# Kernel optimization log

Measured on AMD Instinct MI355X. Metric: run time of the kernel, lower is better.

The kernel has to match this reference:

```python
import jax, jax.numpy as jnp
import numpy as np

NU, NI, E = 100000, 100000, 500000  # users, items, edges per edge type
DIN, DH, DOUT = 128, 256, 128


def setup_inputs() -> dict:
    key = jax.random.key(0)
    ks = jax.random.split(key, 18)
    f = lambda k, s: jax.random.normal(k, s, dtype=jnp.float32) * 0.02
    inp = {
        # node embedding tables (x_dict defaults to embedding weights)
        'emb_user': f(ks[0], (NU, DIN)),
        'emb_item': f(ks[1], (NI, DIN)),
        # conv1 params: relation user->item (dst=item) and item->user (dst=user)
        'W1_self_ui': f(ks[2], (DIN, DH)), 'W1_neigh_ui': f(ks[3], (DIN, DH)), 'b1_ui': jnp.zeros((DH,), jnp.float32),
        'W1_self_iu': f(ks[4], (DIN, DH)), 'W1_neigh_iu': f(ks[5], (DIN, DH)), 'b1_iu': jnp.zeros((DH,), jnp.float32),
        # conv2 params
        'W2_self_ui': f(ks[6], (DH, DOUT)), 'W2_neigh_ui': f(ks[7], (DH, DOUT)), 'b2_ui': jnp.zeros((DOUT,), jnp.float32),
        'W2_self_iu': f(ks[8], (DH, DOUT)), 'W2_neigh_iu': f(ks[9], (DH, DOUT)), 'b2_iu': jnp.zeros((DOUT,), jnp.float32),
        # edge lists: e1 = user->item edges, e2 = item->user edges
        'e1_src': jax.random.randint(ks[10], (E,), 0, NU),
        'e1_dst': jax.random.randint(ks[11], (E,), 0, NI),
        'e2_src': jax.random.randint(ks[12], (E,), 0, NI),
        'e2_dst': jax.random.randint(ks[13], (E,), 0, NU),
    }
    return inp


def _sage(h_src, h_dst, e_src, e_dst, W_self, W_neigh, b, n_dst):
    # DGL SAGEConv('mean'): fc_self(h_dst) + fc_neigh(mean_neighbors(h_src)) + bias
    msg = h_src[e_src]                                   # [E, d] gather
    ssum = jax.ops.segment_sum(msg, e_dst, num_segments=n_dst)          # [n_dst, d]
    deg = jax.ops.segment_sum(jnp.ones((e_src.shape[0], 1), h_src.dtype), e_dst, num_segments=n_dst)
    mean = ssum / jnp.maximum(deg, 1.0)                  # zero in-degree -> 0
    return h_dst @ W_self + mean @ W_neigh + b


def reference(emb_user, emb_item,
              W1_self_ui, W1_neigh_ui, b1_ui, W1_self_iu, W1_neigh_iu, b1_iu,
              W2_self_ui, W2_neigh_ui, b2_ui, W2_self_iu, W2_neigh_iu, b2_iu,
              e1_src, e1_dst, e2_src, e2_dst):
    # layer 1 (HeteroGraphConv: each ntype receives from exactly one relation)
    h1_item = jax.nn.leaky_relu(_sage(emb_user, emb_item, e1_src, e1_dst, W1_self_ui, W1_neigh_ui, b1_ui, NI))
    h1_user = jax.nn.leaky_relu(_sage(emb_item, emb_user, e2_src, e2_dst, W1_self_iu, W1_neigh_iu, b1_iu, NU))
    # layer 2
    h2_item = _sage(h1_user, h1_item, e1_src, e1_dst, W2_self_ui, W2_neigh_ui, b2_ui, NI)
    h2_user = _sage(h1_item, h1_user, e2_src, e2_dst, W2_self_iu, W2_neigh_iu, b2_iu, NU)
    return (h2_user, h2_item)
```

## Files before the change

kernel.cpp:

```cpp
#include <hip/hip_runtime.h>
#include <stdint.h>

typedef unsigned short u16;
typedef unsigned int   u32;
typedef __attribute__((ext_vector_type(8))) short bf16x8;
typedef __attribute__((ext_vector_type(4))) float f32x4;
typedef __attribute__((ext_vector_type(2))) float f32x2;
typedef __attribute__((ext_vector_type(8))) unsigned short u16x8;

constexpr int NUc = 100000;
constexpr int NIc = 100000;
constexpr int Ec  = 500000;
constexpr int Mrows = 100000;
constexpr int NB  = (100000 + 255) / 256;

__device__ __forceinline__ u16 f2bf(float f) {
  u32 u = __float_as_uint(f);
  u += 0x7fffu + ((u >> 16) & 1u);
  return (u16)(u >> 16);
}
__device__ __forceinline__ float bf2f(u16 h) { return __uint_as_float(((u32)h) << 16); }

constexpr int PREP_B = 4096;
constexpr int HIST_B = 1024;
__global__ void prep_hist(const float* __restrict__ eu, const float* __restrict__ ei,
                          const float* __restrict__ W1s_ui, const float* __restrict__ W1n_ui,
                          const float* __restrict__ W1s_iu, const float* __restrict__ W1n_iu,
                          const float* __restrict__ W2s_ui, const float* __restrict__ W2n_ui,
                          const float* __restrict__ W2s_iu, const float* __restrict__ W2n_iu,
                          u16* __restrict__ ue, u16* __restrict__ ie,
                          u16* __restrict__ Wt1_ui, u16* __restrict__ Wt1_iu,
                          u16* __restrict__ Wt2c_u, u16* __restrict__ Wt2c_i,
                          const int* __restrict__ e1_dst, const int* __restrict__ e2_dst,
                          int* __restrict__ ideg1, int* __restrict__ ideg2,
                          int* __restrict__ rank1, int* __restrict__ rank2) {
  if (blockIdx.x < PREP_B) {
    constexpr int N4 = NUc * 128 / 4;
    constexpr int TOT = 2 * N4 + 262144;
    int i = blockIdx.x * blockDim.x + threadIdx.x;
    const int stride = PREP_B * 256;
    for (int t = i; t < TOT; t += stride) {
      if (t < 2 * N4) {
        const float* src = (t < N4) ? eu : ei;
        u16* dst = (t < N4) ? ue : ie;
        int c = (t < N4) ? t : t - N4;
        f32x4 v = __builtin_nontemporal_load(reinterpret_cast<const f32x4*>(src) + c);
        ushort4 o;
        o.x = f2bf(v.x); o.y = f2bf(v.y); o.z = f2bf(v.z); o.w = f2bf(v.w);
        reinterpret_cast<ushort4*>(dst)[c] = o;
      } else {
        int j = t - 2 * N4;
        if (j < 131072) {
          const float* Ws = (j < 65536) ? W1s_ui : W1s_iu;
          const float* Wn = (j < 65536) ? W1n_ui : W1n_iu;
          u16* dst = (j < 65536) ? Wt1_ui : Wt1_iu;
          int q = j & 65535;
          int n = q >> 8, k = q & 255;
          dst[q] = f2bf(k < 128 ? Ws[k * 256 + n] : Wn[(k - 128) * 256 + n]);
        } else {
          int q = j - 131072;
          int which = q >> 16;
          int s = q & 65535;
          int c = s >> 8, k = s & 255;
          float v;
          if (which == 0) v = (c < 128) ? W2n_ui[k * 128 + c] : W2s_iu[k * 128 + (c - 128)];
          else            v = (c < 128) ? W2n_iu[k * 128 + c] : W2s_ui[k * 128 + (c - 128)];
          u16* dst = which ? Wt2c_i : Wt2c_u;
          dst[s] = f2bf(v);
        }
      }
    }
  } else {
    int i = (blockIdx.x - PREP_B) * blockDim.x + threadIdx.x;
    const int stride = HIST_B * 256;
    for (; i < 2 * Ec; i += stride) {
      if (i < Ec) rank1[i] = atomicAdd(&ideg1[e1_dst[i]], 1);
      else        rank2[i - Ec] = atomicAdd(&ideg2[e2_dst[i - Ec]], 1);
    }
  }
}

__global__ void block_reduce2(const int* __restrict__ ideg1, const int* __restrict__ ideg2,
                              int* __restrict__ bsum1, int* __restrict__ bsum2, int n) {
  const int* deg = blockIdx.y ? ideg2 : ideg1;
  int* bsum = blockIdx.y ? bsum2 : bsum1;
  __shared__ int s[256];
  int t = threadIdx.x, i = blockIdx.x * 256 + t;
  s[t] = (i < n) ? deg[i] : 0;
  __syncthreads();
  for (int st = 128; st > 0; st >>= 1) { if (t < st) s[t] += s[t + st]; __syncthreads(); }
  if (t == 0) bsum[blockIdx.x] = s[0];
}

__global__ void scan_bsums2(const int* __restrict__ bsum1, const int* __restrict__ bsum2,
                            int* __restrict__ bscan1, int* __restrict__ bscan2, int nb) {
  const int* bsum = blockIdx.x ? bsum2 : bsum1;
  int* bscan = blockIdx.x ? bscan2 : bscan1;
  __shared__ int s[512];
  int t = threadIdx.x;
  int v0 = (t < nb) ? bsum[t] : 0;
  s[t] = v0;
  __syncthreads();
  for (int d = 1; d < 512; d <<= 1) {
    int v = (t >= d) ? s[t - d] : 0;
    __syncthreads();
    s[t] += v;
    __syncthreads();
  }
  if (t < nb) bscan[t] = s[t] - v0;
}

__global__ void scan_blocks2(const int* __restrict__ ideg1, const int* __restrict__ ideg2,
                             const int* __restrict__ bscan1, const int* __restrict__ bscan2,
                             int* __restrict__ off1, int* __restrict__ off2, int n) {
  const int* deg = blockIdx.y ? ideg2 : ideg1;
  const int* bscan = blockIdx.y ? bscan2 : bscan1;
  int* off = blockIdx.y ? off2 : off1;
  __shared__ int s[256];
  int t = threadIdx.x, i = blockIdx.x * 256 + t;
  int d = (i < n) ? deg[i] : 0;
  s[t] = d;
  __syncthreads();
  for (int st = 1; st < 256; st <<= 1) {
    int v = (t >= st) ? s[t - st] : 0;
    __syncthreads();
    s[t] += v;
    __syncthreads();
  }
  if (i < n) off[i] = bscan[blockIdx.x] + s[t] - d;
  if (i == 0) off[n] = Ec;
}

__global__ void fill_csr_kernel(const int* __restrict__ e1_src, const int* __restrict__ e1_dst,
                                const int* __restrict__ e2_src, const int* __restrict__ e2_dst,
                                const int* __restrict__ rank1, const int* __restrict__ rank2,
                                const int* __restrict__ off1, const int* __restrict__ off2,
                                int* __restrict__ csr1, int* __restrict__ csr2) {
  int i = blockIdx.x * blockDim.x + threadIdx.x;
  const int stride = gridDim.x * blockDim.x;
  for (; i < 2 * Ec; i += stride) {
    if (i < Ec) {
      int d = __builtin_nontemporal_load(e1_dst + i);
      int r = __builtin_nontemporal_load(rank1 + i);
      csr1[off1[d] + r] = __builtin_nontemporal_load(e1_src + i);
    } else {
      int e = i - Ec;
      int d = __builtin_nontemporal_load(e2_dst + e);
      int r = __builtin_nontemporal_load(rank2 + e);
      csr2[off2[d] + r] = __builtin_nontemporal_load(e2_src + e);
    }
  }
}

__global__ __launch_bounds__(256) void gather2(const u16* __restrict__ fA, const int* __restrict__ offA,
                                               const int* __restrict__ csrA, u16* __restrict__ outA,
                                               const u16* __restrict__ fB, const int* __restrict__ offB,
                                               const int* __restrict__ csrB, u16* __restrict__ outB) {
  const int wid  = (blockIdx.x * blockDim.x + threadIdx.x) >> 6;
  const int lane = threadIdx.x & 63;
  const u16* f; const int* off; const int* csr; u16* out; int r;
  if (wid < 100000)      { f = fA; off = offA; csr = csrA; out = outA; r = wid; }
  else if (wid < 200000) { f = fB; off = offB; csr = csrB; out = outB; r = wid - 100000; }
  else return;
  const int j0 = off[r], j1 = off[r + 1];
  const int colb = lane << 1;
  float ax = 0.f, ay = 0.f;
  for (int jb = j0; jb < j1; jb += 64) {
    int cnt = min(64, j1 - jb);
    int idx = (jb + lane < j1) ? csr[jb + lane] : 0;
    int t = 0;
    for (; t + 4 <= cnt; t += 4) {
      int s0 = __shfl(idx, t),     s1 = __shfl(idx, t + 1);
      int s2 = __shfl(idx, t + 2), s3 = __shfl(idx, t + 3);
      u32 v0 = *reinterpret_cast<const u32*>(f + (size_t)s0 * 128 + colb);
      u32 v1 = *reinterpret_cast<const u32*>(f + (size_t)s1 * 128 + colb);
      u32 v2 = *reinterpret_cast<const u32*>(f + (size_t)s2 * 128 + colb);
      u32 v3 = *reinterpret_cast<const u32*>(f + (size_t)s3 * 128 + colb);
      ax += __uint_as_float(v0 << 16) + __uint_as_float(v1 << 16)
          + __uint_as_float(v2 << 16) + __uint_as_float(v3 << 16);
      ay += __uint_as_float(v0 & 0xffff0000u) + __uint_as_float(v1 & 0xffff0000u)
          + __uint_as_float(v2 & 0xffff0000u) + __uint_as_float(v3 & 0xffff0000u);
    }
    for (; t < cnt; ++t) {
      int s0 = __shfl(idx, t);
      u32 v0 = *reinterpret_cast<const u32*>(f + (size_t)s0 * 128 + colb);
      ax += __uint_as_float(v0 << 16);
      ay += __uint_as_float(v0 & 0xffff0000u);
    }
  }
  float rs = 1.0f / fmaxf((float)(j1 - j0), 1.0f);
  u32 o = (u32)f2bf(ax * rs) | ((u32)f2bf(ay * rs) << 16);
  *reinterpret_cast<u32*>(out + (size_t)r * 128 + colb) = o;
}

__global__ __launch_bounds__(256) void gather_final(
    const u16* __restrict__ pA, const int* __restrict__ offA, const int* __restrict__ csrA,
    const u16* __restrict__ sA, float* __restrict__ oA,
    const u16* __restrict__ pB, const int* __restrict__ offB, const int* __restrict__ csrB,
    const u16* __restrict__ sB, float* __restrict__ oB) {
  const int wid  = (blockIdx.x * blockDim.x + threadIdx.x) >> 6;
  const int lane = threadIdx.x & 63;
  const u16* f; const int* off; const int* csr; const u16* sf; float* out; int r;
  if (wid < 100000)      { f = pA; off = offA; csr = csrA; sf = sA; out = oA; r = wid; }
  else if (wid < 200000) { f = pB; off = offB; csr = csrB; sf = sB; out = oB; r = wid - 100000; }
  else return;
  const int j0 = off[r], j1 = off[r + 1];
  const int colb = lane << 1;
  float ax = 0.f, ay = 0.f;
  for (int jb = j0; jb < j1; jb += 64) {
    int cnt = min(64, j1 - jb);
    int idx = (jb + lane < j1) ? csr[jb + lane] : 0;
    int t = 0;
    for (; t + 4 <= cnt; t += 4) {
      int s0 = __shfl(idx, t),     s1 = __shfl(idx, t + 1);
      int s2 = __shfl(idx, t + 2), s3 = __shfl(idx, t + 3);
      u32 v0 = *reinterpret_cast<const u32*>(f + (size_t)s0 * 128 + colb);
      u32 v1 = *reinterpret_cast<const u32*>(f + (size_t)s1 * 128 + colb);
      u32 v2 = *reinterpret_cast<const u32*>(f + (size_t)s2 * 128 + colb);
      u32 v3 = *reinterpret_cast<const u32*>(f + (size_t)s3 * 128 + colb);
      ax += __uint_as_float(v0 << 16) + __uint_as_float(v1 << 16)
          + __uint_as_float(v2 << 16) + __uint_as_float(v3 << 16);
      ay += __uint_as_float(v0 & 0xffff0000u) + __uint_as_float(v1 & 0xffff0000u)
          + __uint_as_float(v2 & 0xffff0000u) + __uint_as_float(v3 & 0xffff0000u);
    }
    for (; t < cnt; ++t) {
      int s0 = __shfl(idx, t);
      u32 v0 = *reinterpret_cast<const u32*>(f + (size_t)s0 * 128 + colb);
      ax += __uint_as_float(v0 << 16);
      ay += __uint_as_float(v0 & 0xffff0000u);
    }
  }
  float rs = 1.0f / fmaxf((float)(j1 - j0), 1.0f);
  u32 sv = __builtin_nontemporal_load(reinterpret_cast<const u32*>(sf + (size_t)r * 128 + colb));
  f32x2 o;
  o.x = ax * rs + __uint_as_float(sv << 16);
  o.y = ay * rs + __uint_as_float(sv & 0xffff0000u);
  __builtin_nontemporal_store(o, reinterpret_cast<f32x2*>(out + (size_t)r * 128 + colb));
}

__device__ __forceinline__ void glds16(const void* g, void* l) {
  __builtin_amdgcn_global_load_lds((const __attribute__((address_space(1))) void*)g,
                                   (__attribute__((address_space(3))) void*)l, 16, 0, 0);
}

template<int NTAB, int EPI, int AST>
__global__ __launch_bounds__(256) void mfma_gemm2(
    const u16* __restrict__ A0a, const u16* __restrict__ A1a, const u16* __restrict__ Bta,
    const float* __restrict__ biasa, u16* __restrict__ out0a, u16* __restrict__ out1a,
    const u16* __restrict__ A0b, const u16* __restrict__ A1b, const u16* __restrict__ Btb,
    const float* __restrict__ biasb, u16* __restrict__ out0b, u16* __restrict__ out1b,
    int M)
{
  constexpr int K = 256, BK = 32, BM = 128;
  __shared__ __align__(16) u16 smem[8192];
  u16* As = smem;
  u16* Bs = smem + 4096;

  const bool zb = (blockIdx.z != 0);
  const u16* A0 = zb ? A0b : A0a;
  const u16* A1 = zb ? A1b : A1a;
  const u16* Bt = zb ? Btb : Bta;
  const float* bias = zb ? biasb : biasa;

  const int tid  = threadIdx.x;
  const int lane = tid & 63;
  const int w    = tid >> 6;
  const int wr   = w >> 1, wc = w & 1;
  const int gr0  = blockIdx.x * BM;
  const int gc0  = blockIdx.y * BM;

  f32x4 acc[4][4];
  #pragma unroll
  for (int m = 0; m < 4; ++m)
    #pragma unroll
    for (int n = 0; n < 4; ++n) acc[m][n] = (f32x4){0.f, 0.f, 0.f, 0.f};

  const int srow  = lane >> 2;
  const int sslot = lane & 3;

  for (int kt = 0; kt < K; kt += BK) {
    const u16* At = (NTAB == 2 && kt >= 128) ? A1 : A0;
    const int kbase = (NTAB == 2) ? (kt & 127) : kt;
    #pragma unroll
    for (int c = 0; c < 2; ++c) {
      int rl = w * 32 + c * 16 + srow;
      int swz = (sslot ^ ((rl >> 1) & 3)) << 3;
      int grow = gr0 + rl; grow = grow < M ? grow : M - 1;
      glds16(At + (size_t)grow * AST + kbase + swz, As + (size_t)(w * 32 + c * 16) * BK);
      glds16(Bt + (size_t)(gc0 + rl) * K + kt + swz, Bs + (size_t)(w * 32 + c * 16) * BK);
    }
    __syncthreads();

    bf16x8 af[4], bfr[4];
    #pragma unroll
    for (int m = 0; m < 4; ++m) {
      int row = wr * 64 + m * 16 + (lane & 15);
      int idx = (row << 5) + ((((lane >> 4) ^ ((row >> 1) & 3))) << 3);
      af[m] = *reinterpret_cast<const bf16x8*>(As + idx);
    }
    #pragma unroll
    for (int n = 0; n < 4; ++n) {
      int row = wc * 64 + n * 16 + (lane & 15);
      int idx = (row << 5) + ((((lane >> 4) ^ ((row >> 1) & 3))) << 3);
      bfr[n] = *reinterpret_cast<const bf16x8*>(Bs + idx);
    }
    #pragma unroll
    for (int m = 0; m < 4; ++m)
      #pragma unroll
      for (int n = 0; n < 4; ++n)
        acc[m][n] = __builtin_amdgcn_mfma_f32_16x16x32_bf16(af[m], bfr[n], acc[m][n], 0, 0, 0);
    __syncthreads();
  }

  u16* outp;
  if (EPI == 0) outp = zb ? out0b : out0a;
  else          outp = (blockIdx.y == 0) ? (zb ? out0b : out0a) : (zb ? out1b : out1a);
  const bool useBias = (EPI == 0) || (blockIdx.y == 1);
  const bool ntStore = (EPI == 1) && (blockIdx.y == 1);

  const int cLane = lane & 15;
  const int rGrp  = (lane >> 4) << 2;
  for (int s = 0; s < 2; ++s) {
    if (wr == s) {
      #pragma unroll
      for (int n = 0; n < 4; ++n) {
        int lc = wc * 64 + n * 16 + cLane;
        float b = 0.f;
        if (useBias) b = (EPI == 0) ? bias[gc0 + lc] : bias[lc];
        #pragma unroll
        for (int m = 0; m < 4; ++m) {
          int lr = m * 16 + rGrp;
          #pragma unroll
          for (int r = 0; r < 4; ++r) {
            float v = acc[m][n][r] + b;
            if (EPI == 0) v = (v >= 0.f) ? v : 0.01f * v;
            smem[(lr + r) * 128 + lc] = f2bf(v);
          }
        }
      }
    }
    __syncthreads();
    #pragma unroll
    for (int pass = 0; pass < 4; ++pass) {
      int chunk = pass * 256 + tid;
      int row = chunk >> 4, c8 = chunk & 15;
      int G = gr0 + s * 64 + row;
      if (G < M) {
        u16x8 v = *reinterpret_cast<const u16x8*>(smem + row * 128 + c8 * 8);
        if (EPI == 0)
          *reinterpret_cast<u16x8*>(outp + (size_t)G * 256 + gc0 + c8 * 8) = v;
        else if (ntStore)
          __builtin_nontemporal_store(v, reinterpret_cast<u16x8*>(outp + (size_t)G * 128 + c8 * 8));
        else
          *reinterpret_cast<u16x8*>(outp + (size_t)G * 128 + c8 * 8) = v;
      }
    }
    if (s == 0) __syncthreads();
  }
}

extern "C" void kernel_launch(void* const* d_in, const int* in_sizes, int n_in,
                              void* d_out, int out_size, void* d_ws, size_t ws_size,
                              hipStream_t stream) {
  const float* emb_user    = (const float*)d_in[0];
  const float* emb_item    = (const float*)d_in[1];
  const float* W1_self_ui  = (const float*)d_in[2];
  const float* W1_neigh_ui = (const float*)d_in[3];
  const float* b1_ui       = (const float*)d_in[4];
  const float* W1_self_iu  = (const float*)d_in[5];
  const float* W1_neigh_iu = (const float*)d_in[6];
  const float* b1_iu       = (const float*)d_in[7];
  const float* W2_self_ui  = (const float*)d_in[8];
  const float* W2_neigh_ui = (const float*)d_in[9];
  const float* b2_ui       = (const float*)d_in[10];
  const float* W2_self_iu  = (const float*)d_in[11];
  const float* W2_neigh_iu = (const float*)d_in[12];
  const float* b2_iu       = (const float*)d_in[13];
  const int* e1_src = (const int*)d_in[14];
  const int* e1_dst = (const int*)d_in[15];
  const int* e2_src = (const int*)d_in[16];
  const int* e2_dst = (const int*)d_in[17];

  u16* p16 = (u16*)d_ws;
  u16* ue     = p16; p16 += (size_t)NUc * 128;
  u16* ie     = p16; p16 += (size_t)NIc * 128;
  u16* h1i    = p16; p16 += (size_t)NIc * 256;
  u16* h1u    = p16; p16 += (size_t)NUc * 256;
  u16* aggb_i = p16; p16 += (size_t)NIc * 128;
  u16* aggb_u = p16; p16 += (size_t)NUc * 128;
  u16* proj_i2u = p16; p16 += (size_t)NIc * 128;
  u16* self_i   = p16; p16 += (size_t)NIc * 128;
  u16* Wt1_ui  = p16; p16 += 256 * 256;
  u16* Wt1_iu  = p16; p16 += 256 * 256;
  u16* Wt2c_u  = p16; p16 += 256 * 256;
  u16* Wt2c_i  = p16; p16 += 256 * 256;
  u16* proj_u2i = aggb_i;
  u16* self_u   = aggb_u;
  int* ip    = (int*)p16;
  int* ideg1 = ip;  ip += NIc;
  int* ideg2 = ip;  ip += NUc;
  int* off1  = ip;  ip += NIc + 1;
  int* off2  = ip;  ip += NUc + 1;
  int* rank1 = ip;  ip += Ec;
  int* rank2 = ip;  ip += Ec;
  int* csr1  = ip;  ip += Ec;
  int* csr2  = ip;  ip += Ec;
  int* bsum1 = ip;  ip += 512;
  int* bscan1= ip;  ip += 512;
  int* bsum2 = ip;  ip += 512;
  int* bscan2= ip;  ip += 512;

  float* h2_user = (float*)d_out;
  float* h2_item = h2_user + (size_t)NUc * 128;

  dim3 blk(256);
  const int gather2Blocks = (200000 + 3) / 4;
  dim3 gemmGrid(782, 2, 2);

  hipMemsetAsync(ideg1, 0, sizeof(int) * (size_t)(NIc + NUc), stream);
  prep_hist<<<PREP_B + HIST_B, blk, 0, stream>>>(
      emb_user, emb_item,
      W1_self_ui, W1_neigh_ui, W1_self_iu, W1_neigh_iu,
      W2_self_ui, W2_neigh_ui, W2_self_iu, W2_neigh_iu,
      ue, ie, Wt1_ui, Wt1_iu, Wt2c_u, Wt2c_i,
      e1_dst, e2_dst, ideg1, ideg2, rank1, rank2);
  block_reduce2<<<dim3(NB, 2), blk, 0, stream>>>(ideg1, ideg2, bsum1, bsum2, NIc);
  scan_bsums2<<<2, 512, 0, stream>>>(bsum1, bsum2, bscan1, bscan2, NB);
  scan_blocks2<<<dim3(NB, 2), blk, 0, stream>>>(ideg1, ideg2, bscan1, bscan2, off1, off2, NIc);
  fill_csr_kernel<<<1024, blk, 0, stream>>>(e1_src, e1_dst, e2_src, e2_dst,
                                            rank1, rank2, off1, off2, csr1, csr2);

  gather2<<<gather2Blocks, blk, 0, stream>>>(ue, off1, csr1, aggb_i,
                                             ie, off2, csr2, aggb_u);
  mfma_gemm2<2, 0, 128><<<gemmGrid, blk, 0, stream>>>(
      ie, aggb_i, Wt1_ui, b1_ui, h1i, nullptr,
      ue, aggb_u, Wt1_iu, b1_iu, h1u, nullptr, Mrows);

  mfma_gemm2<1, 1, 256><<<gemmGrid, blk, 0, stream>>>(
      h1u, nullptr, Wt2c_u, b2_iu, proj_u2i, self_u,
      h1i, nullptr, Wt2c_i, b2_ui, proj_i2u, self_i, Mrows);

  gather_final<<<gather2Blocks, blk, 0, stream>>>(
      proj_u2i, off1, csr1, self_i, h2_item,
      proj_i2u, off2, csr2, self_u, h2_user);
}
```

Before: 365.4 us.

## Widen GEMM tiles to full 256 columns with 512-thread blocks; reorder hist blocks first

The MFMA GEMM now uses 512-thread blocks that compute all 256 output columns per 128-row tile. Before, two column blocks each reloaded the same A rows, so this halves A-tile traffic and the grid's y dimension. The epilogue now runs in four staged passes through shared memory, which adds syncs and a larger LDS footprint. Separately, the atomic histogram blocks are placed ahead of the conversion blocks in the fused prep kernel so the atomic work is scheduled first.

```diff
diff --git a/kernel.cpp b/kernel.cpp
--- a/kernel.cpp
+++ b/kernel.cpp
@@ -34,10 +34,17 @@
                           const int* __restrict__ e1_dst, const int* __restrict__ e2_dst,
                           int* __restrict__ ideg1, int* __restrict__ ideg2,
                           int* __restrict__ rank1, int* __restrict__ rank2) {
-  if (blockIdx.x < PREP_B) {
+  if (blockIdx.x < HIST_B) {
+    int i = blockIdx.x * blockDim.x + threadIdx.x;
+    const int stride = HIST_B * 256;
+    for (; i < 2 * Ec; i += stride) {
+      if (i < Ec) rank1[i] = atomicAdd(&ideg1[e1_dst[i]], 1);
+      else        rank2[i - Ec] = atomicAdd(&ideg2[e2_dst[i - Ec]], 1);
+    }
+  } else {
     constexpr int N4 = NUc * 128 / 4;
     constexpr int TOT = 2 * N4 + 262144;
-    int i = blockIdx.x * blockDim.x + threadIdx.x;
+    int i = (blockIdx.x - HIST_B) * blockDim.x + threadIdx.x;
     const int stride = PREP_B * 256;
     for (int t = i; t < TOT; t += stride) {
       if (t < 2 * N4) {
@@ -70,13 +77,6 @@
         }
       }
     }
-  } else {
-    int i = (blockIdx.x - PREP_B) * blockDim.x + threadIdx.x;
-    const int stride = HIST_B * 256;
-    for (; i < 2 * Ec; i += stride) {
-      if (i < Ec) rank1[i] = atomicAdd(&ideg1[e1_dst[i]], 1);
-      else        rank2[i - Ec] = atomicAdd(&ideg2[e2_dst[i - Ec]], 1);
-    }
   }
 }
 
@@ -244,7 +244,7 @@
 }
 
 template<int NTAB, int EPI, int AST>
-__global__ __launch_bounds__(256) void mfma_gemm2(
+__global__ __launch_bounds__(512) void mfma_gemm2(
     const u16* __restrict__ A0a, const u16* __restrict__ A1a, const u16* __restrict__ Bta,
     const float* __restrict__ biasa, u16* __restrict__ out0a, u16* __restrict__ out1a,
     const u16* __restrict__ A0b, const u16* __restrict__ A1b, const u16* __restrict__ Btb,
@@ -252,7 +252,7 @@
     int M)
 {
   constexpr int K = 256, BK = 32, BM = 128;
-  __shared__ __align__(16) u16 smem[8192];
+  __shared__ __align__(16) u16 smem[12288];
   u16* As = smem;
   u16* Bs = smem + 4096;
 
@@ -265,9 +265,8 @@
   const int tid  = threadIdx.x;
   const int lane = tid & 63;
   const int w    = tid >> 6;
-  const int wr   = w >> 1, wc = w & 1;
+  const int wr   = w >> 2, wc = w & 3;
   const int gr0  = blockIdx.x * BM;
-  const int gc0  = blockIdx.y * BM;
 
   f32x4 acc[4][4];
   #pragma unroll
@@ -281,13 +280,17 @@
   for (int kt = 0; kt < K; kt += BK) {
     const u16* At = (NTAB == 2 && kt >= 128) ? A1 : A0;
     const int kbase = (NTAB == 2) ? (kt & 127) : kt;
+    {
+      int ra = w * 16 + srow;
+      int swz = (sslot ^ ((ra >> 1) & 3)) << 3;
+      int grow = gr0 + ra; grow = grow < M ? grow : M - 1;
+      glds16(At + (size_t)grow * AST + kbase + swz, As + (size_t)(w * 16) * BK);
+    }
     #pragma unroll
     for (int c = 0; c < 2; ++c) {
-      int rl = w * 32 + c * 16 + srow;
-      int swz = (sslot ^ ((rl >> 1) & 3)) << 3;
-      int grow = gr0 + rl; grow = grow < M ? grow : M - 1;
-      glds16(At + (size_t)grow * AST + kbase + swz, As + (size_t)(w * 32 + c * 16) * BK);
-      glds16(Bt + (size_t)(gc0 + rl) * K + kt + swz, Bs + (size_t)(w * 32 + c * 16) * BK);
+      int rb = w * 32 + c * 16 + srow;
+      int swz = (sslot ^ ((rb >> 1) & 3)) << 3;
+      glds16(Bt + (size_t)rb * K + kt + swz, Bs + (size_t)(w * 32 + c * 16) * BK);
     }
     __syncthreads();
 
@@ -312,21 +315,18 @@
     __syncthreads();
   }
 
-  u16* outp;
-  if (EPI == 0) outp = zb ? out0b : out0a;
-  else          outp = (blockIdx.y == 0) ? (zb ? out0b : out0a) : (zb ? out1b : out1a);
-  const bool useBias = (EPI == 0) || (blockIdx.y == 1);
-  const bool ntStore = (EPI == 1) && (blockIdx.y == 1);
-
   const int cLane = lane & 15;
   const int rGrp  = (lane >> 4) << 2;
-  for (int s = 0; s < 2; ++s) {
-    if (wr == s) {
+  #pragma unroll
+  for (int rd = 0; rd < 4; ++rd) {
+    const int s = rd >> 1, ch = rd & 1;
+    if (wr == s && (wc >> 1) == ch) {
       #pragma unroll
       for (int n = 0; n < 4; ++n) {
-        int lc = wc * 64 + n * 16 + cLane;
+        int lc = (wc & 1) * 64 + n * 16 + cLane;
         float b = 0.f;
-        if (useBias) b = (EPI == 0) ? bias[gc0 + lc] : bias[lc];
+        if (EPI == 0) b = bias[ch * 128 + lc];
+        else if (ch == 1) b = bias[lc];
         #pragma unroll
         for (int m = 0; m < 4; ++m) {
           int lr = m * 16 + rGrp;
@@ -341,21 +341,25 @@
     }
     __syncthreads();
     #pragma unroll
-    for (int pass = 0; pass < 4; ++pass) {
-      int chunk = pass * 256 + tid;
+    for (int pass = 0; pass < 2; ++pass) {
+      int chunk = pass * 512 + tid;
       int row = chunk >> 4, c8 = chunk & 15;
       int G = gr0 + s * 64 + row;
       if (G < M) {
         u16x8 v = *reinterpret_cast<const u16x8*>(smem + row * 128 + c8 * 8);
-        if (EPI == 0)
-          *reinterpret_cast<u16x8*>(outp + (size_t)G * 256 + gc0 + c8 * 8) = v;
-        else if (ntStore)
+        if (EPI == 0) {
+          u16* outp = zb ? out0b : out0a;
+          *reinterpret_cast<u16x8*>(outp + (size_t)G * 256 + ch * 128 + c8 * 8) = v;
+        } else if (ch == 0) {
+          u16* outp = zb ? out0b : out0a;
+          *reinterpret_cast<u16x8*>(outp + (size_t)G * 128 + c8 * 8) = v;
+        } else {
+          u16* outp = zb ? out1b : out1a;
           __builtin_nontemporal_store(v, reinterpret_cast<u16x8*>(outp + (size_t)G * 128 + c8 * 8));
-        else
-          *reinterpret_cast<u16x8*>(outp + (size_t)G * 128 + c8 * 8) = v;
+        }
       }
     }
-    if (s == 0) __syncthreads();
+    if (rd < 3) __syncthreads();
   }
 }
 
@@ -414,11 +418,12 @@
   float* h2_item = h2_user + (size_t)NUc * 128;
 
   dim3 blk(256);
+  dim3 blk512(512);
   const int gather2Blocks = (200000 + 3) / 4;
-  dim3 gemmGrid(782, 2, 2);
+  dim3 gemmGrid(782, 1, 2);
 
   hipMemsetAsync(ideg1, 0, sizeof(int) * (size_t)(NIc + NUc), stream);
-  prep_hist<<<PREP_B + HIST_B, blk, 0, stream>>>(
+  prep_hist<<<HIST_B + PREP_B, blk, 0, stream>>>(
       emb_user, emb_item,
       W1_self_ui, W1_neigh_ui, W1_self_iu, W1_neigh_iu,
       W2_self_ui, W2_neigh_ui, W2_self_iu, W2_neigh_iu,
@@ -432,11 +437,11 @@
 
   gather2<<<gather2Blocks, blk, 0, stream>>>(ue, off1, csr1, aggb_i,
                                              ie, off2, csr2, aggb_u);
-  mfma_gemm2<2, 0, 128><<<gemmGrid, blk, 0, stream>>>(
+  mfma_gemm2<2, 0, 128><<<gemmGrid, blk512, 0, stream>>>(
       ie, aggb_i, Wt1_ui, b1_ui, h1i, nullptr,
       ue, aggb_u, Wt1_iu, b1_iu, h1u, nullptr, Mrows);
 
-  mfma_gemm2<1, 1, 256><<<gemmGrid, blk, 0, stream>>>(
+  mfma_gemm2<1, 1, 256><<<gemmGrid, blk512, 0, stream>>>(
       h1u, nullptr, Wt2c_u, b2_iu, proj_u2i, self_u,
       h1i, nullptr, Wt2c_i, b2_ui, proj_i2u, self_i, Mrows);
 
```

Measured after the change: 397.1 us. 8.7% more time.

## Stage per-block CSR slices in LDS and process 64 rows per block

Applied to the files above, without the earlier changes.

Replaces the one-wave-per-row gather kernels with a templated block kernel where each 256-thread block handles 64 consecutive destination rows. The block loads the row offsets and the contiguous CSR index slice into shared memory once, then each wave walks its rows reading neighbor indices from LDS instead of shuffling per-wave global loads. The aim is fewer global index loads and less launch and wave overhead per row. The trade-offs are extra syncthreads, a global fallback path for oversized slices, and only four waves per block, each walking 16 rows serially, which may reduce memory-level parallelism.

```diff
diff --git a/kernel.cpp b/kernel.cpp
--- a/kernel.cpp
+++ b/kernel.cpp
@@ -152,90 +152,96 @@
   }
 }
 
-__global__ __launch_bounds__(256) void gather2(const u16* __restrict__ fA, const int* __restrict__ offA,
-                                               const int* __restrict__ csrA, u16* __restrict__ outA,
-                                               const u16* __restrict__ fB, const int* __restrict__ offB,
-                                               const int* __restrict__ csrB, u16* __restrict__ outB) {
-  const int wid  = (blockIdx.x * blockDim.x + threadIdx.x) >> 6;
-  const int lane = threadIdx.x & 63;
-  const u16* f; const int* off; const int* csr; u16* out; int r;
-  if (wid < 100000)      { f = fA; off = offA; csr = csrA; out = outA; r = wid; }
-  else if (wid < 200000) { f = fB; off = offB; csr = csrB; out = outB; r = wid - 100000; }
-  else return;
-  const int j0 = off[r], j1 = off[r + 1];
+template<int FINAL>
+__global__ __launch_bounds__(256) void gather_blk(
+    const u16* __restrict__ fA, const int* __restrict__ offA, const int* __restrict__ csrA,
+    const u16* __restrict__ sA, void* __restrict__ outA,
+    const u16* __restrict__ fB, const int* __restrict__ offB, const int* __restrict__ csrB,
+    const u16* __restrict__ sB, void* __restrict__ outB)
+{
+  constexpr int ROWS = 64;
+  constexpr int CAP  = 1536;
+  constexpr int NBLK = (100000 + ROWS - 1) / ROWS;
+  __shared__ int s_off[ROWS + 1];
+  __shared__ int s_csr[CAP];
+
+  const int b = blockIdx.x;
+  const u16* f; const int* off; const int* csr; const u16* sf; void* out; int r0;
+  if (b < NBLK) { f = fA; off = offA; csr = csrA; sf = sA; out = outA; r0 = b * ROWS; }
+  else          { f = fB; off = offB; csr = csrB; sf = sB; out = outB; r0 = (b - NBLK) * ROWS; }
+
+  const int tid = threadIdx.x;
+  if (tid <= ROWS) s_off[tid] = off[min(r0 + tid, 100000)];
+  __syncthreads();
+  const int j0 = s_off[0];
+  const int nE = s_off[ROWS] - j0;
+  const bool inLds = (nE <= CAP);
+  if (inLds) {
+    for (int j = tid; j < nE; j += 256) s_csr[j] = csr[j0 + j];
+  }
+  __syncthreads();
+
+  const int w = tid >> 6, lane = tid & 63;
   const int colb = lane << 1;
-  float ax = 0.f, ay = 0.f;
-  for (int jb = j0; jb < j1; jb += 64) {
-    int cnt = min(64, j1 - jb);
-    int idx = (jb + lane < j1) ? csr[jb + lane] : 0;
-    int t = 0;
-    for (; t + 4 <= cnt; t += 4) {
-      int s0 = __shfl(idx, t),     s1 = __shfl(idx, t + 1);
-      int s2 = __shfl(idx, t + 2), s3 = __shfl(idx, t + 3);
-      u32 v0 = *reinterpret_cast<const u32*>(f + (size_t)s0 * 128 + colb);
-      u32 v1 = *reinterpret_cast<const u32*>(f + (size_t)s1 * 128 + colb);
-      u32 v2 = *reinterpret_cast<const u32*>(f + (size_t)s2 * 128 + colb);
-      u32 v3 = *reinterpret_cast<const u32*>(f + (size_t)s3 * 128 + colb);
-      ax += __uint_as_float(v0 << 16) + __uint_as_float(v1 << 16)
-          + __uint_as_float(v2 << 16) + __uint_as_float(v3 << 16);
-      ay += __uint_as_float(v0 & 0xffff0000u) + __uint_as_float(v1 & 0xffff0000u)
-          + __uint_as_float(v2 & 0xffff0000u) + __uint_as_float(v3 & 0xffff0000u);
-    }
-    for (; t < cnt; ++t) {
-      int s0 = __shfl(idx, t);
-      u32 v0 = *reinterpret_cast<const u32*>(f + (size_t)s0 * 128 + colb);
-      ax += __uint_as_float(v0 << 16);
-      ay += __uint_as_float(v0 & 0xffff0000u);
-    }
-  }
-  float rs = 1.0f / fmaxf((float)(j1 - j0), 1.0f);
-  u32 o = (u32)f2bf(ax * rs) | ((u32)f2bf(ay * rs) << 16);
-  *reinterpret_cast<u32*>(out + (size_t)r * 128 + colb) = o;
-}
-
-__global__ __launch_bounds__(256) void gather_final(
-    const u16* __restrict__ pA, const int* __restrict__ offA, const int* __restrict__ csrA,
-    const u16* __restrict__ sA, float* __restrict__ oA,
-    const u16* __restrict__ pB, const int* __restrict__ offB, const int* __restrict__ csrB,
-    const u16* __restrict__ sB, float* __restrict__ oB) {
-  const int wid  = (blockIdx.x * blockDim.x + threadIdx.x) >> 6;
-  const int lane = threadIdx.x & 63;
-  const u16* f; const int* off; const int* csr; const u16* sf; float* out; int r;
-  if (wid < 100000)      { f = pA; off = offA; csr = csrA; sf = sA; out = oA; r = wid; }
-  else if (wid < 200000) { f = pB; off = offB; csr = csrB; sf = sB; out = oB; r = wid - 100000; }
-  else return;
-  const int j0 = off[r], j1 = off[r + 1];
-  const int colb = lane << 1;
-  float ax = 0.f, ay = 0.f;
-  for (int jb = j0; jb < j1; jb += 64) {
-    int cnt = min(64, j1 - jb);
-    int idx = (jb + lane < j1) ? csr[jb + lane] : 0;
-    int t = 0;
-    for (; t + 4 <= cnt; t += 4) {
-      int s0 = __shfl(idx, t),     s1 = __shfl(idx, t + 1);
-      int s2 = __shfl(idx, t + 2), s3 = __shfl(idx, t + 3);
-      u32 v0 = *reinterpret_cast<const u32*>(f + (size_t)s0 * 128 + colb);
-      u32 v1 = *reinterpret_cast<const u32*>(f + (size_t)s1 * 128 + colb);
-      u32 v2 = *reinterpret_cast<const u32*>(f + (size_t)s2 * 128 + colb);
-      u32 v3 = *reinterpret_cast<const u32*>(f + (size_t)s3 * 128 + colb);
-      ax += __uint_as_float(v0 << 16) + __uint_as_float(v1 << 16)
-          + __uint_as_float(v2 << 16) + __uint_as_float(v3 << 16);
-      ay += __uint_as_float(v0 & 0xffff0000u) + __uint_as_float(v1 & 0xffff0000u)
-          + __uint_as_float(v2 & 0xffff0000u) + __uint_as_float(v3 & 0xffff0000u);
-    }
-    for (; t < cnt; ++t) {
-      int s0 = __shfl(idx, t);
-      u32 v0 = *reinterpret_cast<const u32*>(f + (size_t)s0 * 128 + colb);
-      ax += __uint_as_float(v0 << 16);
-      ay += __uint_as_float(v0 & 0xffff0000u);
-    }
-  }
-  float rs = 1.0f / fmaxf((float)(j1 - j0), 1.0f);
-  u32 sv = __builtin_nontemporal_load(reinterpret_cast<const u32*>(sf + (size_t)r * 128 + colb));
-  f32x2 o;
-  o.x = ax * rs + __uint_as_float(sv << 16);
-  o.y = ay * rs + __uint_as_float(sv & 0xffff0000u);
-  __builtin_nontemporal_store(o, reinterpret_cast<f32x2*>(out + (size_t)r * 128 + colb));
+  for (int rr = w; rr < ROWS; rr += 4) {
+    const int r = r0 + rr;
+    if (r >= 100000) break;
+    const int a0 = s_off[rr], a1 = s_off[rr + 1];
+    float ax = 0.f, ay = 0.f;
+    int t = a0;
+    if (inLds) {
+      const int base = a0 - j0;
+      int tl = base;
+      const int el = a1 - j0;
+      for (; tl + 4 <= el; tl += 4) {
+        int s0 = s_csr[tl], s1 = s_csr[tl + 1], s2 = s_csr[tl + 2], s3 = s_csr[tl + 3];
+        u32 v0 = *reinterpret_cast<const u32*>(f + (size_t)s0 * 128 + colb);
+        u32 v1 = *reinterpret_cast<const u32*>(f + (size_t)s1 * 128 + colb);
+        u32 v2 = *reinterpret_cast<const u32*>(f + (size_t)s2 * 128 + colb);
+        u32 v3 = *reinterpret_cast<const u32*>(f + (size_t)s3 * 128 + colb);
+        ax += __uint_as_float(v0 << 16) + __uint_as_float(v1 << 16)
+            + __uint_as_float(v2 << 16) + __uint_as_float(v3 << 16);
+        ay += __uint_as_float(v0 & 0xffff0000u) + __uint_as_float(v1 & 0xffff0000u)
+            + __uint_as_float(v2 & 0xffff0000u) + __uint_as_float(v3 & 0xffff0000u);
+      }
+      for (; tl < el; ++tl) {
+        int s0 = s_csr[tl];
+        u32 v0 = *reinterpret_cast<const u32*>(f + (size_t)s0 * 128 + colb);
+        ax += __uint_as_float(v0 << 16);
+        ay += __uint_as_float(v0 & 0xffff0000u);
+      }
+    } else {
+      for (; t + 4 <= a1; t += 4) {
+        int s0 = csr[t], s1 = csr[t + 1], s2 = csr[t + 2], s3 = csr[t + 3];
+        u32 v0 = *reinterpret_cast<const u32*>(f + (size_t)s0 * 128 + colb);
+        u32 v1 = *reinterpret_cast<const u32*>(f + (size_t)s1 * 128 + colb);
+        u32 v2 = *reinterpret_cast<const u32*>(f + (size_t)s2 * 128 + colb);
+        u32 v3 = *reinterpret_cast<const u32*>(f + (size_t)s3 * 128 + colb);
+        ax += __uint_as_float(v0 << 16) + __uint_as_float(v1 << 16)
+            + __uint_as_float(v2 << 16) + __uint_as_float(v3 << 16);
+        ay += __uint_as_float(v0 & 0xffff0000u) + __uint_as_float(v1 & 0xffff0000u)
+            + __uint_as_float(v2 & 0xffff0000u) + __uint_as_float(v3 & 0xffff0000u);
+      }
+      for (; t < a1; ++t) {
+        int s0 = csr[t];
+        u32 v0 = *reinterpret_cast<const u32*>(f + (size_t)s0 * 128 + colb);
+        ax += __uint_as_float(v0 << 16);
+        ay += __uint_as_float(v0 & 0xffff0000u);
+      }
+    }
+    float rs = 1.0f / fmaxf((float)(a1 - a0), 1.0f);
+    if (FINAL) {
+      u32 sv = __builtin_nontemporal_load(
+          reinterpret_cast<const u32*>(sf + (size_t)r * 128 + colb));
+      f32x2 o;
+      o.x = ax * rs + __uint_as_float(sv << 16);
+      o.y = ay * rs + __uint_as_float(sv & 0xffff0000u);
+      __builtin_nontemporal_store(o, reinterpret_cast<f32x2*>((float*)out + (size_t)r * 128 + colb));
+    } else {
+      u32 o = (u32)f2bf(ax * rs) | ((u32)f2bf(ay * rs) << 16);
+      *reinterpret_cast<u32*>((u16*)out + (size_t)r * 128 + colb) = o;
+    }
+  }
 }
 
 __device__ __forceinline__ void glds16(const void* g, void* l) {
@@ -414,7 +420,7 @@
   float* h2_item = h2_user + (size_t)NUc * 128;
 
   dim3 blk(256);
-  const int gather2Blocks = (200000 + 3) / 4;
+  const int gatherBlocks = 2 * ((100000 + 63) / 64);
   dim3 gemmGrid(782, 2, 2);
 
   hipMemsetAsync(ideg1, 0, sizeof(int) * (size_t)(NIc + NUc), stream);
@@ -430,8 +436,9 @@
   fill_csr_kernel<<<1024, blk, 0, stream>>>(e1_src, e1_dst, e2_src, e2_dst,
                                             rank1, rank2, off1, off2, csr1, csr2);
 
-  gather2<<<gather2Blocks, blk, 0, stream>>>(ue, off1, csr1, aggb_i,
-                                             ie, off2, csr2, aggb_u);
+  gather_blk<0><<<gatherBlocks, blk, 0, stream>>>(
+      ue, off1, csr1, nullptr, aggb_i,
+      ie, off2, csr2, nullptr, aggb_u);
   mfma_gemm2<2, 0, 128><<<gemmGrid, blk, 0, stream>>>(
       ie, aggb_i, Wt1_ui, b1_ui, h1i, nullptr,
       ue, aggb_u, Wt1_iu, b1_iu, h1u, nullptr, Mrows);
@@ -440,7 +447,7 @@
       h1u, nullptr, Wt2c_u, b2_iu, proj_u2i, self_u,
       h1i, nullptr, Wt2c_i, b2_ui, proj_i2u, self_i, Mrows);
 
-  gather_final<<<gather2Blocks, blk, 0, stream>>>(
+  gather_blk<1><<<gatherBlocks, blk, 0, stream>>>(
       proj_u2i, off1, csr1, self_i, h2_item,
       proj_i2u, off2, csr2, self_u, h2_user);
 }
```

New measurement: 345.5 us. -5.4%, faster.
